# Performance work log

Measured on AMD Instinct MI355X. Metric: run time of the kernel, lower is better.

The kernel has to match this reference:

```python
import jax, jax.numpy as jnp
import numpy as np

TEMPERATURE = 0.5
N_NODES = 100000
N_EDGES = 3200000
D = 32


def setup_inputs() -> dict:
    key = jax.random.key(0)
    ks = jax.random.split(key, 8)
    node_reps = jax.random.normal(ks[0], (N_NODES, D), dtype=jnp.float32)
    edge_reps = jax.random.normal(ks[1], (N_EDGES, D), dtype=jnp.float32)
    graph_rep = jax.random.normal(ks[2], (D,), dtype=jnp.float32)
    subgraph_rep = jax.random.normal(ks[3], (D,), dtype=jnp.float32)
    W = jax.random.normal(ks[4], (3 * D, D), dtype=jnp.float32) / np.sqrt(3 * D)
    b = jax.random.normal(ks[5], (D,), dtype=jnp.float32) * 0.01
    edge_index = jax.random.randint(ks[6], (2, N_EDGES), 0, N_NODES, dtype=jnp.int64)
    selection = jax.random.randint(ks[7], (N_EDGES,), 0, 2) > 0
    return {
        "node_reps": node_reps,
        "edge_reps": edge_reps,
        "graph_rep": graph_rep,
        "subgraph_rep": subgraph_rep,
        "W": W,
        "b": b,
        "edge_index": edge_index,
        "selection": selection,
    }


def reference(node_reps, edge_reps, graph_rep, subgraph_rep, W, b, edge_index, selection):
    # Gather endpoint node reps per edge: [E, 32] each
    src = node_reps[edge_index[0]]
    dst = node_reps[edge_index[1]]
    # Concat -> [E, 96], Linear + ELU -> [E, 32]
    h = jnp.concatenate([src, dst, edge_reps], axis=1)
    edge_action_reps = jax.nn.elu(h @ W + b)
    # State scores: [E] = [E,32] @ [32]
    state_prob = edge_action_reps @ (graph_rep - subgraph_rep)
    # Mask already-selected edges to the global minimum, then softmax with temperature
    min_prob = jnp.min(state_prob)
    state_prob = jnp.where(selection, min_prob, state_prob)
    return jax.nn.softmax(state_prob[None, :] / TEMPERATURE, axis=1)
```

## Files before the change

kernel.cpp:

```cpp
#include <hip/hip_runtime.h>
#include <hip/hip_bf16.h>
#include <stdint.h>

#define DD 32
#define KH 96


__device__ __forceinline__ uint32_t fkey(float f) {
    uint32_t b = __float_as_uint(f);
    return (b & 0x80000000u) ? ~b : (b | 0x80000000u);
}
__device__ __forceinline__ float funkey(uint32_t k) {
    uint32_t b = (k & 0x80000000u) ? (k & 0x7FFFFFFFu) : ~k;
    return __uint_as_float(b);
}
__device__ __forceinline__ float bflo(uint32_t w) { return __uint_as_float(w << 16); }
__device__ __forceinline__ float bfhi(uint32_t w) { return __uint_as_float(w & 0xFFFF0000u); }
__device__ __forceinline__ uint16_t f2bf(float v) {
    uint32_t u = __float_as_uint(v);
    uint32_t r = (u + 0x7FFFu + ((u >> 16) & 1u)) >> 16;
    return (uint16_t)r;
}

__global__ void k_init(const void* W, const void* bias, const void* g, const void* sg,
                       const void* ei, const void* sel,
                       uint32_t* hdr, float* Wf, float* bf, float* vf, int E, int N) {
    int t = threadIdx.x;
    __shared__ int sh_i32, sh_gt1, sh_odd, sh_f32;
    if (t == 0) { sh_i32 = 0; sh_gt1 = 0; sh_odd = 0; sh_f32 = 0; }
    __syncthreads();

    const uint16_t* wb = (const uint16_t*)W;
    for (int i = t; i < KH * DD; i += 256) {
        float x = bflo((uint32_t)wb[i]);
        if (!(fabsf(x) < 1e4f)) sh_f32 = 1;
    }
    const long long* ell = (const long long*)ei;
    int ns = 2048 < E ? 2048 : E;
    for (int i = t; i < ns; i += 256) {
        long long v = ell[i];
        if (v < 0 || v >= (long long)N) sh_i32 = 1;
    }
    const uint32_t* sw = (const uint32_t*)sel;
    int ns2 = 2048 < E / 4 ? 2048 : E / 4;
    for (int i = t; i < ns2; i += 256) {
        uint32_t v = sw[i];
        if (v > 1u) sh_gt1 = 1;
        if (v != 0u && (i & 1)) sh_odd = 1;
    }
    __syncthreads();
    int fmode = sh_f32;

    for (int i = t; i < KH * DD; i += 256)
        Wf[i] = fmode ? ((const float*)W)[i] : bflo((uint32_t)wb[i]);
    for (int i = t; i < DD; i += 256) {
        bf[i] = fmode ? ((const float*)bias)[i] : bflo((uint32_t)((const uint16_t*)bias)[i]);
        float gv = fmode ? ((const float*)g)[i]  : bflo((uint32_t)((const uint16_t*)g)[i]);
        float sv = fmode ? ((const float*)sg)[i] : bflo((uint32_t)((const uint16_t*)sg)[i]);
        vf[i] = gv - sv;
    }
    if (t == 0) {
        hdr[0] = (uint32_t)sh_i32;
        hdr[1] = sh_gt1 ? 2u : (sh_odd ? 1u : 0u);
        hdr[2] = (uint32_t)fmode;
        hdr[3] = 0xFFFFFFFFu;
        hdr[4] = 0u;
        hdr[5] = 0u;
        hdr[6] = 0u;
    }
}

__device__ __forceinline__ void loadrow(const char* __restrict__ p, int fmode, float* h) {
    if (fmode) {
        const float4* q = (const float4*)p;
        #pragma unroll
        for (int t = 0; t < 8; ++t) {
            float4 u = q[t];
            h[t * 4 + 0] = u.x; h[t * 4 + 1] = u.y; h[t * 4 + 2] = u.z; h[t * 4 + 3] = u.w;
        }
    } else {
        const uint4* q = (const uint4*)p;
        #pragma unroll
        for (int t = 0; t < 4; ++t) {
            uint4 u = q[t];
            h[t * 8 + 0] = bflo(u.x); h[t * 8 + 1] = bfhi(u.x);
            h[t * 8 + 2] = bflo(u.y); h[t * 8 + 3] = bfhi(u.y);
            h[t * 8 + 4] = bflo(u.z); h[t * 8 + 5] = bfhi(u.z);
            h[t * 8 + 6] = bflo(u.w); h[t * 8 + 7] = bfhi(u.w);
        }
    }
}

__device__ __forceinline__ bool fetch_sel(const char* sel, int mode, int e) {
    if (mode == 2) return ((const uint8_t*)sel)[e] != 0;
    if (mode == 1) return ((const int*)sel)[e] != 0;
    return ((const long long*)sel)[e] != 0;
}

__device__ __forceinline__ void sp_store(float* __restrict__ ws_sp, void* __restrict__ out,
                                         int use_ws, int fmode, int e, float v) {
    if (use_ws) ws_sp[e] = v;
    else if (fmode) ((float*)out)[e] = v;
    else ((uint16_t*)out)[e] = f2bf(v);
}
__device__ __forceinline__ float sp_load(const float* __restrict__ ws_sp, const void* __restrict__ out,
                                         int use_ws, int fmode, int e) {
    if (use_ws) return ws_sp[e];
    if (fmode) return ((const float*)out)[e];
    return bflo((uint32_t)((const uint16_t*)out)[e]);
}

__global__ __launch_bounds__(256) void k_pass1(
    const char* __restrict__ node, const char* __restrict__ edgep,
    const char* __restrict__ ei, const char* __restrict__ sel,
    uint32_t* __restrict__ hdr, const float* __restrict__ Wf,
    const float* __restrict__ bf, const float* __restrict__ vf,
    float* __restrict__ ws_sp, void* __restrict__ out,
    int use_ws, int E, int N) {
    __shared__ __align__(16) float Ws[KH * DD];
    __shared__ float bs[DD], vs[DD];
    for (int i = threadIdx.x; i < KH * DD; i += 256) Ws[i] = Wf[i];
    if (threadIdx.x < DD) { bs[threadIdx.x] = bf[threadIdx.x]; vs[threadIdx.x] = vf[threadIdx.x]; }
    const int idx_mode = (int)hdr[0];
    const int sel_mode = (int)hdr[1];
    const int fmode    = (int)hdr[2];
    __syncthreads();

    int e = blockIdx.x * 256 + threadIdx.x;
    bool valid = e < E;
    int ec = valid ? e : E - 1;

    long long si, di;
    if (idx_mode) { si = ((const int*)ei)[ec]; di = ((const int*)ei)[E + ec]; }
    else          { si = ((const long long*)ei)[ec]; di = ((const long long*)ei)[(size_t)E + ec]; }
    int s0 = (int)si; s0 = s0 < 0 ? 0 : (s0 >= N ? N - 1 : s0);
    int d0 = (int)di; d0 = d0 < 0 ? 0 : (d0 >= N ? N - 1 : d0);

    size_t rb = fmode ? 128 : 64;
    const char* p0 = node  + (size_t)s0 * rb;
    const char* p1 = node  + (size_t)d0 * rb;
    const char* p2 = edgep + (size_t)ec * rb;

    float acc[DD];
    #pragma unroll
    for (int j = 0; j < DD; ++j) acc[j] = bs[j];

    float hh[32], hn[32];
    loadrow(p0, fmode, hh);

    #pragma unroll 1
    for (int r = 0; r < 3; ++r) {
        if (r < 2) {
            const char* pn = (r == 0) ? p1 : p2;
            loadrow(pn, fmode, hn);
        }
        const float* wb = &Ws[r * 32 * DD];
        #pragma unroll
        for (int k = 0; k < 32; ++k) {
            float hk = hh[k];
            const float4* wp = (const float4*)(wb + k * DD);
            #pragma unroll
            for (int j4 = 0; j4 < 8; ++j4) {
                float4 w = wp[j4];
                acc[j4 * 4 + 0] = fmaf(hk, w.x, acc[j4 * 4 + 0]);
                acc[j4 * 4 + 1] = fmaf(hk, w.y, acc[j4 * 4 + 1]);
                acc[j4 * 4 + 2] = fmaf(hk, w.z, acc[j4 * 4 + 2]);
                acc[j4 * 4 + 3] = fmaf(hk, w.w, acc[j4 * 4 + 3]);
            }
        }
        if (r < 2) {
            #pragma unroll
            for (int k = 0; k < 32; ++k) hh[k] = hn[k];
        }
    }

    float sp = 0.f;
    #pragma unroll
    for (int j = 0; j < DD; ++j) {
        float a = acc[j];
        float act = a > 0.f ? a : (__expf(a) - 1.f);
        sp = fmaf(act, vs[j], sp);
    }

    bool selv = true;
    if (valid) {
        sp_store(ws_sp, out, use_ws, fmode, e, sp);
        selv = fetch_sel(sel, sel_mode, e);
    }

    float mn = valid ? sp : __builtin_inff();
    float mx = (valid && !selv) ? sp : -__builtin_inff();
    uint32_t c = (valid && !selv) ? 1u : 0u;
    #pragma unroll
    for (int o = 32; o >= 1; o >>= 1) {
        mn = fminf(mn, __shfl_xor(mn, o));
        mx = fmaxf(mx, __shfl_xor(mx, o));
        c += __shfl_xor(c, o);
    }
    __shared__ float smn[4], smx[4];
    __shared__ uint32_t sc[4];
    int wid = threadIdx.x >> 6, lane = threadIdx.x & 63;
    if (lane == 0) { smn[wid] = mn; smx[wid] = mx; sc[wid] = c; }
    __syncthreads();
    if (threadIdx.x == 0) {
        for (int w = 1; w < 4; ++w) { mn = fminf(mn, smn[w]); mx = fmaxf(mx, smx[w]); c += sc[w]; }
        atomicMin(&hdr[3], fkey(mn));
        atomicMax(&hdr[4], fkey(mx));
        if (c) atomicAdd(&hdr[5], c);
    }
}

__global__ __launch_bounds__(256) void k_pass2(
    const char* __restrict__ sel, uint32_t* __restrict__ hdr,
    const float* __restrict__ ws_sp, const void* __restrict__ out,
    int use_ws, int E) {
    int e = blockIdx.x * 256 + threadIdx.x;
    int sel_mode = (int)hdr[1], fmode = (int)hdr[2];
    float mn = funkey(hdr[3]);
    uint32_t cnt = hdr[5];
    float M = cnt ? funkey(hdr[4]) : mn;
    float p = 0.f;
    if (e < E) {
        float sp = sp_load(ws_sp, out, use_ws, fmode, e);
        bool selv = fetch_sel(sel, sel_mode, e);
        float masked = selv ? mn : sp;
        p = __expf((masked - M) * 2.0f);
    }
    #pragma unroll
    for (int o = 32; o >= 1; o >>= 1) p += __shfl_xor(p, o);
    __shared__ float sps[4];
    int wid = threadIdx.x >> 6, lane = threadIdx.x & 63;
    if (lane == 0) sps[wid] = p;
    __syncthreads();
    if (threadIdx.x == 0) {
        p += sps[1] + sps[2] + sps[3];
        atomicAdd((float*)&hdr[6], p);
    }
}

__global__ __launch_bounds__(256) void k_pass3(
    const char* __restrict__ sel, const uint32_t* __restrict__ hdr,
    const float* __restrict__ ws_sp, void* __restrict__ out,
    int use_ws, int E) {
    int e = blockIdx.x * 256 + threadIdx.x;
    if (e >= E) return;
    int sel_mode = (int)hdr[1], fmode = (int)hdr[2];
    float mn = funkey(hdr[3]);
    uint32_t cnt = hdr[5];
    float M = cnt ? funkey(hdr[4]) : mn;
    float S = __uint_as_float(hdr[6]);
    float sp = sp_load(ws_sp, out, use_ws, fmode, e);
    bool selv = fetch_sel(sel, sel_mode, e);
    float masked = selv ? mn : sp;
    float r = __expf((masked - M) * 2.0f) / S;
    if (fmode) ((float*)out)[e] = r;
    else       ((uint16_t*)out)[e] = f2bf(r);
}

extern "C" void kernel_launch(void* const* d_in, const int* in_sizes, int n_in,
                              void* d_out, int out_size, void* d_ws, size_t ws_size,
                              hipStream_t stream) {
    int N = in_sizes[0] / DD;
    int E = in_sizes[1] / DD;
    const void* node = d_in[0];
    const void* edge = d_in[1];
    const void* g    = d_in[2];
    const void* sg   = d_in[3];
    const void* W    = d_in[4];
    const void* bias = d_in[5];
    const void* ei   = d_in[6];
    const void* sel  = d_in[7];

    uint8_t* ws = (uint8_t*)d_ws;
    uint32_t* hdr = (uint32_t*)ws;
    float* Wf = (float*)(ws + 256);
    float* bf = (float*)(ws + 256 + 12288);
    float* vf = (float*)(ws + 256 + 12288 + 128);
    float* sp_arr = (float*)(ws + 16384);
    int use_ws = (ws_size >= (size_t)16384 + (size_t)E * sizeof(float)) ? 1 : 0;

    int grid = (E + 255) / 256;
    k_init<<<1, 256, 0, stream>>>(W, bias, g, sg, ei, sel, hdr, Wf, bf, vf, E, N);
    k_pass1<<<grid, 256, 0, stream>>>((const char*)node, (const char*)edge, (const char*)ei,
                                      (const char*)sel, hdr, Wf, bf, vf, sp_arr, d_out,
                                      use_ws, E, N);
    k_pass2<<<grid, 256, 0, stream>>>((const char*)sel, hdr, sp_arr, d_out, use_ws, E);
    k_pass3<<<grid, 256, 0, stream>>>((const char*)sel, hdr, sp_arr, d_out, use_ws, E);
}
```

Measured before the change: 1.142 ms.

## Read weights via scalar loads into SGPRs instead of LDS staging

Removes the shared-memory copy of W, bias and the score vector, and the block barrier that guarded it. The weights are now read per k-row with s_load_dwordx16 into scalar registers, so the FMAs take SGPR operands in place of LDS reads. The cost is a full lgkmcnt(0) wait inside the unrolled loop, which serializes scalar memory latency with the math. It also raises SGPR pressure and relies on the wave-uniform pointer being 64-byte aligned for the scalar loads.

```diff
diff --git a/kernel.cpp b/kernel.cpp
--- a/kernel.cpp
+++ b/kernel.cpp
@@ -5,6 +5,8 @@
 #define DD 32
 #define KH 96
 
+
+typedef __attribute__((ext_vector_type(16))) float vf16;
 
 __device__ __forceinline__ uint32_t fkey(float f) {
     uint32_t b = __float_as_uint(f);
@@ -20,6 +22,14 @@
     uint32_t u = __float_as_uint(v);
     uint32_t r = (u + 0x7FFFu + ((u >> 16) & 1u)) >> 16;
     return (uint16_t)r;
+}
+
+__device__ __forceinline__ void wload(const float* p, vf16& a, vf16& b) {
+    asm volatile("s_load_dwordx16 %0, %2, 0x0\n\t"
+                 "s_load_dwordx16 %1, %2, 0x40\n\t"
+                 "s_waitcnt lgkmcnt(0)"
+                 : "=&s"(a), "=&s"(b)
+                 : "s"(p));
 }
 
 __global__ void k_init(const void* W, const void* bias, const void* g, const void* sg,
@@ -117,14 +127,9 @@
     const float* __restrict__ bf, const float* __restrict__ vf,
     float* __restrict__ ws_sp, void* __restrict__ out,
     int use_ws, int E, int N) {
-    __shared__ __align__(16) float Ws[KH * DD];
-    __shared__ float bs[DD], vs[DD];
-    for (int i = threadIdx.x; i < KH * DD; i += 256) Ws[i] = Wf[i];
-    if (threadIdx.x < DD) { bs[threadIdx.x] = bf[threadIdx.x]; vs[threadIdx.x] = vf[threadIdx.x]; }
     const int idx_mode = (int)hdr[0];
     const int sel_mode = (int)hdr[1];
     const int fmode    = (int)hdr[2];
-    __syncthreads();
 
     int e = blockIdx.x * 256 + threadIdx.x;
     bool valid = e < E;
@@ -142,8 +147,12 @@
     const char* p2 = edgep + (size_t)ec * rb;
 
     float acc[DD];
-    #pragma unroll
-    for (int j = 0; j < DD; ++j) acc[j] = bs[j];
+    {
+        vf16 b0, b1;
+        wload(bf, b0, b1);
+        #pragma unroll
+        for (int j = 0; j < 16; ++j) { acc[j] = b0[j]; acc[16 + j] = b1[j]; }
+    }
 
     float hh[32], hn[32];
     loadrow(p0, fmode, hh);
@@ -154,18 +163,16 @@
             const char* pn = (r == 0) ? p1 : p2;
             loadrow(pn, fmode, hn);
         }
-        const float* wb = &Ws[r * 32 * DD];
+        const float* wp = Wf + r * 32 * DD;
         #pragma unroll
         for (int k = 0; k < 32; ++k) {
+            vf16 w0, w1;
+            wload(wp + k * DD, w0, w1);
             float hk = hh[k];
-            const float4* wp = (const float4*)(wb + k * DD);
             #pragma unroll
-            for (int j4 = 0; j4 < 8; ++j4) {
-                float4 w = wp[j4];
-                acc[j4 * 4 + 0] = fmaf(hk, w.x, acc[j4 * 4 + 0]);
-                acc[j4 * 4 + 1] = fmaf(hk, w.y, acc[j4 * 4 + 1]);
-                acc[j4 * 4 + 2] = fmaf(hk, w.z, acc[j4 * 4 + 2]);
-                acc[j4 * 4 + 3] = fmaf(hk, w.w, acc[j4 * 4 + 3]);
+            for (int j = 0; j < 16; ++j) {
+                acc[j]      = fmaf(hk, w0[j], acc[j]);
+                acc[16 + j] = fmaf(hk, w1[j], acc[16 + j]);
             }
         }
         if (r < 2) {
@@ -175,11 +182,18 @@
     }
 
     float sp = 0.f;
-    #pragma unroll
-    for (int j = 0; j < DD; ++j) {
-        float a = acc[j];
-        float act = a > 0.f ? a : (__expf(a) - 1.f);
-        sp = fmaf(act, vs[j], sp);
+    {
+        vf16 v0, v1;
+        wload(vf, v0, v1);
+        #pragma unroll
+        for (int j = 0; j < 16; ++j) {
+            float a = acc[j];
+            float act = a > 0.f ? a : (__expf(a) - 1.f);
+            sp = fmaf(act, v0[j], sp);
+            float a2 = acc[16 + j];
+            float act2 = a2 > 0.f ? a2 : (__expf(a2) - 1.f);
+            sp = fmaf(act2, v1[j], sp);
+        }
     }
 
     bool selv = true;
```

Measured after the change: 1.126 ms. Within noise of the previous version (-1.4%).
